# Optimization experiments

Hardware: AMD Instinct MI355X
Metric: run time of the kernel (lower is better)

## Reference

```python
import jax, jax.numpy as jnp
import numpy as np

D, H, E, K, DF = 1024, 16, 8, 2, 4096
HD = D // H


def setup_inputs() -> dict:
    key = jax.random.key(0)
    ks = jax.random.split(key, 16)
    s = 0.02
    return {
        "x": jax.random.normal(ks[0], (8, 1024, D), jnp.float32),
        "ln1_g": jnp.ones((D,), jnp.float32),
        "ln1_b": jnp.zeros((D,), jnp.float32),
        "Wqkv": jax.random.normal(ks[1], (D, 3 * D), jnp.float32) * s,
        "bqkv": jnp.zeros((3 * D,), jnp.float32),
        "Wo": jax.random.normal(ks[2], (D, D), jnp.float32) * s,
        "bo": jnp.zeros((D,), jnp.float32),
        "ln2_g": jnp.ones((D,), jnp.float32),
        "ln2_b": jnp.zeros((D,), jnp.float32),
        "Wr": jax.random.normal(ks[3], (D, E), jnp.float32) * s,
        "W1": jax.random.normal(ks[4], (E, D, DF), jnp.float32) * s,
        "b1": jnp.zeros((E, DF), jnp.float32),
        "W2": jax.random.normal(ks[5], (E, DF, D), jnp.float32) * s,
        "b2": jnp.zeros((E, D), jnp.float32),
    }


def _ln(x, g, b, eps=1e-5):
    mu = jnp.mean(x, axis=-1, keepdims=True)
    var = jnp.var(x, axis=-1, keepdims=True)
    return (x - mu) * jax.lax.rsqrt(var + eps) * g + b


def reference(x, ln1_g, ln1_b, Wqkv, bqkv, Wo, bo, ln2_g, ln2_b, Wr, W1, b1, W2, b2):
    B, S, _ = x.shape
    # ---- pre-norm multi-head attention ----
    n1 = _ln(x, ln1_g, ln1_b)
    qkv = n1 @ Wqkv + bqkv  # [B,S,3D]
    q, k, v = jnp.split(qkv, 3, axis=-1)
    q = q.reshape(B, S, H, HD).transpose(0, 2, 1, 3)
    k = k.reshape(B, S, H, HD).transpose(0, 2, 1, 3)
    v = v.reshape(B, S, H, HD).transpose(0, 2, 1, 3)
    scores = jnp.einsum("bhqd,bhkd->bhqk", q, k) / np.sqrt(HD).astype(np.float32)
    attn = jax.nn.softmax(scores, axis=-1)
    ao = jnp.einsum("bhqk,bhkd->bhqd", attn, v)
    ao = ao.transpose(0, 2, 1, 3).reshape(B, S, D) @ Wo + bo
    x = x + ao  # residual (dropout=0)

    # ---- pre-norm MoE FFN ----
    n2 = _ln(x, ln2_g, ln2_b).reshape(B * S, D)  # [T,D]
    logits = n2 @ Wr  # [T,E]
    probs = jax.nn.softmax(logits, axis=-1)
    topv, topi = jax.lax.top_k(probs, K)  # [T,K]
    topv = topv / jnp.sum(topv, axis=-1, keepdims=True)
    onehot = jax.nn.one_hot(topi, E, dtype=probs.dtype)  # [T,K,E]
    gates = jnp.einsum("tke,tk->te", onehot, topv)  # dense sparse gates [T,E]

    # dense dispatch: each expert's FFN weighted by its gate (zero for unrouted)
    moe = jnp.zeros_like(n2)
    for e in range(E):
        h = jax.nn.gelu(n2 @ W1[e] + b1[e])
        moe = moe + gates[:, e:e + 1] * (h @ W2[e] + b2[e])
    x = x + moe.reshape(B, S, D)

    # load-balancing aux loss: E * sum(frac_routed_e * mean_prob_e)
    frac = jnp.mean(jnp.sum(onehot, axis=1), axis=0) / K  # [E]
    aux = E * jnp.sum(frac * jnp.mean(probs, axis=0))
    return x, aux
```

## Files before the change

kernel.cpp:

```cpp
#include <hip/hip_runtime.h>
#include <cstdint>
#include <cstddef>

using u16 = unsigned short;
using u32 = unsigned int;
typedef __attribute__((ext_vector_type(8))) short bf16x8;
typedef __attribute__((ext_vector_type(4))) float f32x4;

#define T_TOK 8192
#define SEQ   1024
#define NHEAD 16

__device__ __forceinline__ u16 f2b(float f) {
  u32 u = __float_as_uint(f);
  u32 r = (u + 0x7FFFu + ((u >> 16) & 1u)) >> 16;
  return (u16)r;
}
__device__ __forceinline__ float b2f(u16 u) {
  return __uint_as_float(((u32)u) << 16);
}

__global__ __launch_bounds__(256)
void k_cast_transpose(const float* __restrict__ in, u16* __restrict__ out, int R, int C) {
  __shared__ float tile[32][33];
  int bc = blockIdx.x * 32, br = blockIdx.y * 32;
  size_t bofs = (size_t)blockIdx.z * R * C;
  in += bofs; out += bofs;
  int tx = threadIdx.x, ty = threadIdx.y;
  for (int i = 0; i < 32; i += 8)
    tile[ty + i][tx] = in[(size_t)(br + ty + i) * C + bc + tx];
  __syncthreads();
  for (int i = 0; i < 32; i += 8)
    out[(size_t)(bc + ty + i) * R + br + tx] = f2b(tile[tx][ty + i]);
}

__global__ __launch_bounds__(256)
void k_ln(const float* __restrict__ x, const float* __restrict__ g, const float* __restrict__ b,
          u16* __restrict__ out) {
  int row = blockIdx.x, t = threadIdx.x;
  float4 v = ((const float4*)(x + (size_t)row * 1024))[t];
  float s  = v.x + v.y + v.z + v.w;
  float ss = v.x * v.x + v.y * v.y + v.z * v.z + v.w * v.w;
  for (int d = 1; d < 64; d <<= 1) { s += __shfl_xor(s, d); ss += __shfl_xor(ss, d); }
  __shared__ float sm[8];
  int w = t >> 6, lane = t & 63;
  if (lane == 0) { sm[w] = s; sm[4 + w] = ss; }
  __syncthreads();
  s = sm[0] + sm[1] + sm[2] + sm[3];
  ss = sm[4] + sm[5] + sm[6] + sm[7];
  float mu = s * (1.f / 1024.f);
  float var = ss * (1.f / 1024.f) - mu * mu;
  float inv = rsqrtf(var + 1e-5f);
  float4 gv = ((const float4*)g)[t];
  float4 bv = ((const float4*)b)[t];
  u32 lo = (u32)f2b((v.x - mu) * inv * gv.x + bv.x) | ((u32)f2b((v.y - mu) * inv * gv.y + bv.y) << 16);
  u32 hi = (u32)f2b((v.z - mu) * inv * gv.z + bv.z) | ((u32)f2b((v.w - mu) * inv * gv.w + bv.w) << 16);
  u32* dst = (u32*)(out + (size_t)row * 1024 + t * 4);
  dst[0] = lo; dst[1] = hi;
}

template<int MODE, bool EXPERT, bool GATHER>
__global__ __launch_bounds__(256)
void k_gemm(const u16* __restrict__ A, const u16* __restrict__ BT,
            const float* __restrict__ bias, const float* __restrict__ res,
            void* __restrict__ Cout, int M, int N, int Kd, int ldA,
            const int* __restrict__ off, const int* __restrict__ rows) {
  int nx = gridDim.x;
  int rid = blockIdx.x + nx * (blockIdx.y + gridDim.y * blockIdx.z);
  int z, bx, by;
  if (EXPERT) {
    z = rid & 7;
    int inner = rid >> 3;
    bx = inner % nx;
    by = inner / nx;
  } else {
    z = 0;
    int xcd = rid & 7;
    int inner = rid >> 3;
    bx = inner % nx;
    by = (inner / nx) * 8 + xcd;
  }
  int m_base = 0, M_local = M;
  if (EXPERT) { m_base = off[z]; M_local = off[z + 1] - m_base; }
  if (by * 128 >= M_local) return;
  if (EXPERT) { BT += (size_t)z * N * Kd; bias += (size_t)z * N; }

  __shared__ alignas(1024) u16 As[2][4096];
  __shared__ alignas(1024) u16 Bs[2][4096];

  int t = threadIdx.x;
  int lane = t & 63, w = t >> 6;
  int wm = w >> 1, wn = w & 1;
  int lr = lane & 15;
  int slot = lane >> 4;
  int sx = (slot ^ ((lr >> 1) & 3)) << 3;

  int ssrc = (lane & 3) ^ ((lane >> 3) & 3);
  const u16* aG[2]; const u16* bG[2];
  u16* aL[2]; u16* bL[2];
#pragma unroll
  for (int c = 0; c < 2; c++) {
    int chunk = 2 * w + c;
    int rl = chunk * 16 + (lane >> 2);
    int mr = by * 128 + rl;
    int mc = mr < M_local - 1 ? mr : M_local - 1;
    size_t arow = GATHER ? (size_t)rows[m_base + mc] : (size_t)(m_base + mc);
    aG[c] = A + arow * (size_t)ldA + ssrc * 8;
    bG[c] = BT + (size_t)(bx * 128 + rl) * Kd + ssrc * 8;
    aL[c] = &As[0][chunk * 512];
    bL[c] = &Bs[0][chunk * 512];
  }

  auto stage = [&](int k0, int buf) {
#pragma unroll
    for (int c = 0; c < 2; c++) {
      __builtin_amdgcn_global_load_lds(
          (const __attribute__((address_space(1))) void*)(aG[c] + k0),
          (__attribute__((address_space(3))) void*)(aL[c] + buf * 4096), 16, 0, 0);
      __builtin_amdgcn_global_load_lds(
          (const __attribute__((address_space(1))) void*)(bG[c] + k0),
          (__attribute__((address_space(3))) void*)(bL[c] + buf * 4096), 16, 0, 0);
    }
  };

  f32x4 acc[4][4] = {};

  stage(0, 0);
  __syncthreads();
  int cur = 0;
  for (int k0 = 0; k0 < Kd; k0 += 32) {
    if (k0 + 32 < Kd) stage(k0 + 32, cur ^ 1);
    bf16x8 af[4], bfr[4];
#pragma unroll
    for (int m = 0; m < 4; m++)
      af[m] = *(const bf16x8*)&As[cur][(wm * 64 + m * 16 + lr) * 32 + sx];
#pragma unroll
    for (int n = 0; n < 4; n++)
      bfr[n] = *(const bf16x8*)&Bs[cur][(wn * 64 + n * 16 + lr) * 32 + sx];
#pragma unroll
    for (int m = 0; m < 4; m++)
#pragma unroll
      for (int n = 0; n < 4; n++)
        acc[m][n] = __builtin_amdgcn_mfma_f32_16x16x32_bf16(af[m], bfr[n], acc[m][n], 0, 0, 0);
    __syncthreads();
    cur ^= 1;
  }

  int cr = (lane >> 4) * 4, cc = lane & 15;
#pragma unroll
  for (int m = 0; m < 4; m++) {
    int rl = by * 128 + wm * 64 + m * 16 + cr;
#pragma unroll
    for (int n = 0; n < 4; n++) {
      int col = bx * 128 + wn * 64 + n * 16 + cc;
      float bia = bias[col];
#pragma unroll
      for (int r = 0; r < 4; r++) {
        int rr = rl + r;
        if (rr >= M_local) continue;
        size_t row = (size_t)(m_base + rr);
        float v = acc[m][n][r] + bia;
        if (MODE == 0) {
          ((u16*)Cout)[row * N + col] = f2b(v);
        } else if (MODE == 1) {
          ((float*)Cout)[row * N + col] = v + res[row * N + col];
        } else if (MODE == 2) {
          float u = v + 0.044715f * v * v * v;
          float ge = v / (1.f + __expf(-1.5957691216057308f * u));
          ((u16*)Cout)[row * N + col] = f2b(ge);
        } else {
          ((float*)Cout)[row * N + col] = v;
        }
      }
    }
  }
}

__global__ __launch_bounds__(256)
void k_attn(const u16* __restrict__ qkv, u16* __restrict__ ao) {
  __shared__ u16 Kt[64][72];
  __shared__ u16 Vt[64][72];
  __shared__ u16 Pl[4][16][72];

  int bh = blockIdx.y;
  int b = bh >> 4, h = bh & 15;
  int q0 = blockIdx.x * 64;
  int t = threadIdx.x, lane = t & 63, w = t >> 6;
  int lr = lane & 15, lk = (lane >> 4) * 8;

  int tq = b * SEQ + q0 + w * 16 + lr;
  const u16* qrow = qkv + (size_t)tq * 3072 + h * 64;
  bf16x8 qf[2];
#pragma unroll
  for (int kk = 0; kk < 2; kk++) {
    bf16x8 raw = *(const bf16x8*)(qrow + kk * 32 + lk);
#pragma unroll
    for (int j = 0; j < 8; j++) raw[j] = (short)f2b(b2f((u16)raw[j]) * 0.125f);
    qf[kk] = raw;
  }

  float m[4], l[4];
  f32x4 o[4];
#pragma unroll
  for (int r = 0; r < 4; r++) { m[r] = -1e30f; l[r] = 0.f; }
#pragma unroll
  for (int c = 0; c < 4; c++) o[c] = (f32x4){0.f, 0.f, 0.f, 0.f};

  int key_r = t >> 2;
  int key_c = (t & 3) * 16;

  for (int kv0 = 0; kv0 < SEQ; kv0 += 64) {
    int tk = b * SEQ + kv0 + key_r;
    const u16* krow = qkv + (size_t)tk * 3072 + 1024 + h * 64 + key_c;
    const u16* vrow = qkv + (size_t)tk * 3072 + 2048 + h * 64 + key_c;
    int4 ka = *(const int4*)krow;
    int4 kb = *(const int4*)(krow + 8);
    int4 vv4[2];
    vv4[0] = *(const int4*)vrow;
    vv4[1] = *(const int4*)(vrow + 8);
    const u16* vv = (const u16*)vv4;
    __syncthreads();
    *(int4*)&Kt[key_r][key_c] = ka;
    *(int4*)&Kt[key_r][key_c + 8] = kb;
#pragma unroll
    for (int j = 0; j < 16; j++) Vt[key_c + j][key_r] = vv[j];
    __syncthreads();

    f32x4 s[4];
#pragma unroll
    for (int n = 0; n < 4; n++) {
      s[n] = (f32x4){0.f, 0.f, 0.f, 0.f};
#pragma unroll
      for (int kk = 0; kk < 2; kk++) {
        bf16x8 kf = *(const bf16x8*)&Kt[n * 16 + lr][kk * 32 + lk];
        s[n] = __builtin_amdgcn_mfma_f32_16x16x32_bf16(qf[kk], kf, s[n], 0, 0, 0);
      }
    }
    float alpha[4], rsum[4];
#pragma unroll
    for (int r = 0; r < 4; r++) {
      float mx = fmaxf(fmaxf(s[0][r], s[1][r]), fmaxf(s[2][r], s[3][r]));
#pragma unroll
      for (int d = 1; d < 16; d <<= 1) mx = fmaxf(mx, __shfl_xor(mx, d));
      float mn = fmaxf(m[r], mx);
      alpha[r] = expf(m[r] - mn);
      m[r] = mn;
      rsum[r] = 0.f;
    }
#pragma unroll
    for (int n = 0; n < 4; n++)
#pragma unroll
      for (int r = 0; r < 4; r++) {
        float p = expf(s[n][r] - m[r]);
        rsum[r] += p;
        Pl[w][(lane >> 4) * 4 + r][n * 16 + lr] = f2b(p);
      }
#pragma unroll
    for (int r = 0; r < 4; r++) {
      float rs = rsum[r];
#pragma unroll
      for (int d = 1; d < 16; d <<= 1) rs += __shfl_xor(rs, d);
      l[r] = l[r] * alpha[r] + rs;
#pragma unroll
      for (int c = 0; c < 4; c++) o[c][r] *= alpha[r];
    }
    bf16x8 pa[2];
#pragma unroll
    for (int kk = 0; kk < 2; kk++) pa[kk] = *(const bf16x8*)&Pl[w][lr][kk * 32 + lk];
#pragma unroll
    for (int c = 0; c < 4; c++)
#pragma unroll
      for (int kk = 0; kk < 2; kk++) {
        bf16x8 vf = *(const bf16x8*)&Vt[c * 16 + lr][kk * 32 + lk];
        o[c] = __builtin_amdgcn_mfma_f32_16x16x32_bf16(pa[kk], vf, o[c], 0, 0, 0);
      }
  }

  int cr = (lane >> 4) * 4, cc = lane & 15;
#pragma unroll
  for (int r = 0; r < 4; r++) {
    float invl = 1.f / l[r];
    int trow = b * SEQ + q0 + w * 16 + cr + r;
#pragma unroll
    for (int c = 0; c < 4; c++)
      ao[(size_t)trow * 1024 + h * 64 + c * 16 + cc] = f2b(o[c][r] * invl);
  }
}

__global__ __launch_bounds__(256)
void k_router(const float* __restrict__ x1, const float* __restrict__ g, const float* __restrict__ b,
              const float* __restrict__ Wr, int* __restrict__ topi, float* __restrict__ topv,
              int* __restrict__ cnt_part, float* __restrict__ sp_part) {
  __shared__ int lcnt[8];
  __shared__ float lsp[8];
  int t = threadIdx.x, w = t >> 6, lane = t & 63;
  if (t < 8) { lcnt[t] = 0; lsp[t] = 0.f; }
  __syncthreads();

  float gv[16], bv[16];
#pragma unroll
  for (int i = 0; i < 4; i++) {
    float4 g4 = ((const float4*)g)[lane * 4 + i];
    float4 b4 = ((const float4*)b)[lane * 4 + i];
    gv[i * 4 + 0] = g4.x; gv[i * 4 + 1] = g4.y; gv[i * 4 + 2] = g4.z; gv[i * 4 + 3] = g4.w;
    bv[i * 4 + 0] = b4.x; bv[i * 4 + 1] = b4.y; bv[i * 4 + 2] = b4.z; bv[i * 4 + 3] = b4.w;
  }
  float wr[16][8];
#pragma unroll
  for (int j = 0; j < 16; j++) {
    float4 w0 = ((const float4*)Wr)[(lane * 16 + j) * 2];
    float4 w1 = ((const float4*)Wr)[(lane * 16 + j) * 2 + 1];
    wr[j][0] = w0.x; wr[j][1] = w0.y; wr[j][2] = w0.z; wr[j][3] = w0.w;
    wr[j][4] = w1.x; wr[j][5] = w1.y; wr[j][6] = w1.z; wr[j][7] = w1.w;
  }

  for (int i = 0; i < 8; i++) {
    int row = blockIdx.x * 32 + w * 8 + i;
    const float4* xr = (const float4*)(x1 + (size_t)row * 1024);
    float xv[16];
    float s = 0.f, ss = 0.f;
#pragma unroll
    for (int q = 0; q < 4; q++) {
      float4 v = xr[lane * 4 + q];
      xv[q * 4 + 0] = v.x; xv[q * 4 + 1] = v.y; xv[q * 4 + 2] = v.z; xv[q * 4 + 3] = v.w;
      s += v.x + v.y + v.z + v.w;
      ss += v.x * v.x + v.y * v.y + v.z * v.z + v.w * v.w;
    }
#pragma unroll
    for (int d = 1; d < 64; d <<= 1) { s += __shfl_xor(s, d); ss += __shfl_xor(ss, d); }
    float mu = s * (1.f / 1024.f);
    float var = ss * (1.f / 1024.f) - mu * mu;
    float inv = rsqrtf(var + 1e-5f);
    float p[8] = {};
#pragma unroll
    for (int j = 0; j < 16; j++) {
      float n = (xv[j] - mu) * inv * gv[j] + bv[j];
#pragma unroll
      for (int e = 0; e < 8; e++) p[e] += n * wr[j][e];
    }
#pragma unroll
    for (int e = 0; e < 8; e++)
#pragma unroll
      for (int d = 1; d < 64; d <<= 1) p[e] += __shfl_xor(p[e], d);
    if (lane == 0) {
      float mx = p[0];
#pragma unroll
      for (int e = 1; e < 8; e++) mx = fmaxf(mx, p[e]);
      float ex[8], sum = 0.f;
#pragma unroll
      for (int e = 0; e < 8; e++) { ex[e] = expf(p[e] - mx); sum += ex[e]; }
      float pr[8];
#pragma unroll
      for (int e = 0; e < 8; e++) pr[e] = ex[e] / sum;
      int i0 = 0; float b0 = pr[0];
      for (int e = 1; e < 8; e++) if (pr[e] > b0) { b0 = pr[e]; i0 = e; }
      int i1 = -1; float b1 = -1.f;
      for (int e = 0; e < 8; e++) if (e != i0 && pr[e] > b1) { b1 = pr[e]; i1 = e; }
      float inv2 = 1.f / (b0 + b1);
      topi[row * 2] = i0; topi[row * 2 + 1] = i1;
      topv[row * 2] = b0 * inv2; topv[row * 2 + 1] = b1 * inv2;
      atomicAdd(&lcnt[i0], 1); atomicAdd(&lcnt[i1], 1);
#pragma unroll
      for (int e = 0; e < 8; e++) atomicAdd(&lsp[e], pr[e]);
    }
  }
  __syncthreads();
  if (t < 8) {
    cnt_part[blockIdx.x * 8 + t] = lcnt[t];
    sp_part[blockIdx.x * 8 + t] = lsp[t];
  }
}

__global__ void k_scan_aux(const int* __restrict__ cnt_part, const float* __restrict__ sp_part,
                           int* __restrict__ off, int* __restrict__ cursor, float* __restrict__ aux_out) {
  __shared__ int csum[8];
  __shared__ float ssum[8];
  int t = threadIdx.x;
  int e = t & 7, ch = t >> 3;
  int c = 0; float s = 0.f;
  for (int i = ch * 32; i < ch * 32 + 32; i++) { c += cnt_part[i * 8 + e]; s += sp_part[i * 8 + e]; }
#pragma unroll
  for (int d = 8; d < 64; d <<= 1) { c += __shfl_xor(c, d); s += __shfl_xor(s, d); }
  if (t < 8) { csum[t] = c; ssum[t] = s; }
  __syncthreads();
  if (t == 0) {
    int o = 0;
    for (int q = 0; q < 8; q++) { off[q] = o; cursor[q] = o; o += csum[q]; }
    off[8] = o;
    float aux = 0.f;
    for (int q = 0; q < 8; q++)
      aux += ((float)csum[q] / (float)(T_TOK * 2)) * (ssum[q] / (float)T_TOK);
    aux_out[0] = 8.f * aux;
  }
}

__global__ __launch_bounds__(256)
void k_scatter(const int* __restrict__ topi, int* __restrict__ cursor,
               int* __restrict__ rows, int* __restrict__ slot_of) {
  __shared__ int hist[8];
  __shared__ int base[8];
  int t = threadIdx.x;
  if (t < 8) hist[t] = 0;
  __syncthreads();
  int tok = blockIdx.x * 256 + t;
  int e0 = topi[tok * 2], e1 = topi[tok * 2 + 1];
  int r0 = atomicAdd(&hist[e0], 1);
  int r1 = atomicAdd(&hist[e1], 1);
  __syncthreads();
  if (t < 8) base[t] = atomicAdd(&cursor[t], hist[t]);
  __syncthreads();
  int p0 = base[e0] + r0, p1 = base[e1] + r1;
  rows[p0] = tok; rows[p1] = tok;
  slot_of[tok * 2] = p0; slot_of[tok * 2 + 1] = p1;
}

__global__ __launch_bounds__(256)
void k_combine(const float* __restrict__ x1, const float* __restrict__ out2,
               const int* __restrict__ slot_of, const float* __restrict__ topv,
               float* __restrict__ out) {
  int row = blockIdx.x, t = threadIdx.x;
  int s0 = slot_of[row * 2], s1 = slot_of[row * 2 + 1];
  float w0 = topv[row * 2], w1 = topv[row * 2 + 1];
  float4 a  = ((const float4*)(x1 + (size_t)row * 1024))[t];
  float4 e0 = ((const float4*)(out2 + (size_t)s0 * 1024))[t];
  float4 e1 = ((const float4*)(out2 + (size_t)s1 * 1024))[t];
  float4 r;
  r.x = a.x + w0 * e0.x + w1 * e1.x;
  r.y = a.y + w0 * e0.y + w1 * e1.y;
  r.z = a.z + w0 * e0.z + w1 * e1.z;
  r.w = a.w + w0 * e0.w + w1 * e1.w;
  ((float4*)(out + (size_t)row * 1024))[t] = r;
}

extern "C" void kernel_launch(void* const* d_in, const int* in_sizes, int n_in,
                              void* d_out, int out_size, void* d_ws, size_t ws_size,
                              hipStream_t stream) {
  const float* x    = (const float*)d_in[0];
  const float* ln1g = (const float*)d_in[1];
  const float* ln1b = (const float*)d_in[2];
  const float* Wqkv = (const float*)d_in[3];
  const float* bqkv = (const float*)d_in[4];
  const float* Wo   = (const float*)d_in[5];
  const float* bo   = (const float*)d_in[6];
  const float* ln2g = (const float*)d_in[7];
  const float* ln2b = (const float*)d_in[8];
  const float* Wr   = (const float*)d_in[9];
  const float* W1   = (const float*)d_in[10];
  const float* b1   = (const float*)d_in[11];
  const float* W2   = (const float*)d_in[12];
  const float* b2   = (const float*)d_in[13];
  float* out = (float*)d_out;

  char* wp = (char*)d_ws;
  auto alloc = [&](size_t bytes) -> void* {
    void* p = (void*)wp;
    wp += (bytes + 255) & ~(size_t)255;
    return p;
  };
  u16*   WqkvT = (u16*)alloc((size_t)3072 * 1024 * 2);
  u16*   WoT   = (u16*)alloc((size_t)1024 * 1024 * 2);
  u16*   W1T   = (u16*)alloc((size_t)8 * 4096 * 1024 * 2);
  u16*   W2T   = (u16*)alloc((size_t)8 * 1024 * 4096 * 2);
  u16*   n1    = (u16*)alloc((size_t)8192 * 1024 * 2);
  u16*   qkv   = (u16*)alloc((size_t)8192 * 3072 * 2);
  u16*   aob   = (u16*)alloc((size_t)8192 * 1024 * 2);
  float* x1    = (float*)alloc((size_t)8192 * 1024 * 4);
  u16*   n2b   = (u16*)alloc((size_t)8192 * 1024 * 2);
  u16*   hbuf  = (u16*)alloc((size_t)16384 * 4096 * 2);
  float* out2  = (float*)alloc((size_t)16384 * 1024 * 4);
  int*   topi  = (int*)alloc((size_t)8192 * 2 * 4);
  float* topv  = (float*)alloc((size_t)8192 * 2 * 4);
  int*   rowsl = (int*)alloc((size_t)16384 * 4);
  int*   slot  = (int*)alloc((size_t)16384 * 4);
  int*   cntp  = (int*)alloc((size_t)256 * 8 * 4);
  float* spp   = (float*)alloc((size_t)256 * 8 * 4);
  int*   offs  = (int*)alloc(256);
  int*   curs  = (int*)alloc(256);

  k_cast_transpose<<<dim3(96, 32, 1), dim3(32, 8), 0, stream>>>(Wqkv, WqkvT, 1024, 3072);
  k_cast_transpose<<<dim3(32, 32, 1), dim3(32, 8), 0, stream>>>(Wo, WoT, 1024, 1024);
  k_cast_transpose<<<dim3(128, 32, 8), dim3(32, 8), 0, stream>>>(W1, W1T, 1024, 4096);
  k_cast_transpose<<<dim3(32, 128, 8), dim3(32, 8), 0, stream>>>(W2, W2T, 4096, 1024);

  k_ln<<<8192, 256, 0, stream>>>(x, ln1g, ln1b, n1);
  k_gemm<0, false, false><<<dim3(24, 64, 1), 256, 0, stream>>>(
      n1, WqkvT, bqkv, nullptr, qkv, 8192, 3072, 1024, 1024, nullptr, nullptr);
  k_attn<<<dim3(16, 128), 256, 0, stream>>>(qkv, aob);
  k_gemm<1, false, false><<<dim3(8, 64, 1), 256, 0, stream>>>(
      aob, WoT, bo, x, x1, 8192, 1024, 1024, 1024, nullptr, nullptr);

  k_ln<<<8192, 256, 0, stream>>>(x1, ln2g, ln2b, n2b);
  k_router<<<256, 256, 0, stream>>>(x1, ln2g, ln2b, Wr, topi, topv, cntp, spp);
  k_scan_aux<<<1, 64, 0, stream>>>(cntp, spp, offs, curs, out + 8388608);
  k_scatter<<<32, 256, 0, stream>>>(topi, curs, rowsl, slot);

  k_gemm<2, true, true><<<dim3(32, 64, 8), 256, 0, stream>>>(
      n2b, W1T, b1, nullptr, hbuf, 0, 4096, 1024, 1024, offs, rowsl);
  k_gemm<3, true, false><<<dim3(8, 64, 8), 256, 0, stream>>>(
      hbuf, W2T, b2, nullptr, out2, 0, 1024, 4096, 4096, offs, nullptr);
  k_combine<<<8192, 256, 0, stream>>>(x1, out2, slot, topv, out);
}
```

Measured before the change: 903.2 us.

## Triple-buffer GEMM LDS staging with explicit vmcnt waits and reorder expert tile mapping

Moves the GEMM mainloop from double to triple buffering in LDS. It replaces __syncthreads with raw s_barrier plus explicit s_waitcnt vmcnt counts, so two global-to-LDS loads stay in flight while each tile is computed. It also changes the expert GEMM block mapping so consecutive blocks walk the M dimension first, which changes reuse of expert weight tiles. The cost is more LDS per block, which may lower occupancy, and hand-written wait counts that must match the number of loads issued per stage.

```diff
diff --git a/kernel.cpp b/kernel.cpp
--- a/kernel.cpp
+++ b/kernel.cpp
@@ -65,14 +65,14 @@
             const float* __restrict__ bias, const float* __restrict__ res,
             void* __restrict__ Cout, int M, int N, int Kd, int ldA,
             const int* __restrict__ off, const int* __restrict__ rows) {
-  int nx = gridDim.x;
-  int rid = blockIdx.x + nx * (blockIdx.y + gridDim.y * blockIdx.z);
+  int nx = gridDim.x, ny = gridDim.y;
+  int rid = blockIdx.x + nx * (blockIdx.y + ny * blockIdx.z);
   int z, bx, by;
   if (EXPERT) {
     z = rid & 7;
     int inner = rid >> 3;
-    bx = inner % nx;
-    by = inner / nx;
+    by = inner % ny;
+    bx = inner / ny;
   } else {
     z = 0;
     int xcd = rid & 7;
@@ -85,8 +85,8 @@
   if (by * 128 >= M_local) return;
   if (EXPERT) { BT += (size_t)z * N * Kd; bias += (size_t)z * N; }
 
-  __shared__ alignas(1024) u16 As[2][4096];
-  __shared__ alignas(1024) u16 Bs[2][4096];
+  __shared__ alignas(1024) u16 As[3][4096];
+  __shared__ alignas(1024) u16 Bs[3][4096];
 
   int t = threadIdx.x;
   int lane = t & 63, w = t >> 6;
@@ -97,7 +97,7 @@
 
   int ssrc = (lane & 3) ^ ((lane >> 3) & 3);
   const u16* aG[2]; const u16* bG[2];
-  u16* aL[2]; u16* bL[2];
+  int cofs[2];
 #pragma unroll
   for (int c = 0; c < 2; c++) {
     int chunk = 2 * w + c;
@@ -107,29 +107,26 @@
     size_t arow = GATHER ? (size_t)rows[m_base + mc] : (size_t)(m_base + mc);
     aG[c] = A + arow * (size_t)ldA + ssrc * 8;
     bG[c] = BT + (size_t)(bx * 128 + rl) * Kd + ssrc * 8;
-    aL[c] = &As[0][chunk * 512];
-    bL[c] = &Bs[0][chunk * 512];
-  }
-
-  auto stage = [&](int k0, int buf) {
+    cofs[c] = chunk * 512;
+  }
+
+  auto stage = [&](int s) {
+    int k0 = s * 32;
+    int buf = s % 3;
 #pragma unroll
     for (int c = 0; c < 2; c++) {
       __builtin_amdgcn_global_load_lds(
           (const __attribute__((address_space(1))) void*)(aG[c] + k0),
-          (__attribute__((address_space(3))) void*)(aL[c] + buf * 4096), 16, 0, 0);
+          (__attribute__((address_space(3))) void*)(&As[buf][cofs[c]]), 16, 0, 0);
       __builtin_amdgcn_global_load_lds(
           (const __attribute__((address_space(1))) void*)(bG[c] + k0),
-          (__attribute__((address_space(3))) void*)(bL[c] + buf * 4096), 16, 0, 0);
+          (__attribute__((address_space(3))) void*)(&Bs[buf][cofs[c]]), 16, 0, 0);
     }
   };
 
   f32x4 acc[4][4] = {};
 
-  stage(0, 0);
-  __syncthreads();
-  int cur = 0;
-  for (int k0 = 0; k0 < Kd; k0 += 32) {
-    if (k0 + 32 < Kd) stage(k0 + 32, cur ^ 1);
+  auto compute = [&](int cur) {
     bf16x8 af[4], bfr[4];
 #pragma unroll
     for (int m = 0; m < 4; m++)
@@ -142,9 +139,23 @@
 #pragma unroll
       for (int n = 0; n < 4; n++)
         acc[m][n] = __builtin_amdgcn_mfma_f32_16x16x32_bf16(af[m], bfr[n], acc[m][n], 0, 0, 0);
-    __syncthreads();
-    cur ^= 1;
-  }
+  };
+
+  int nsteps = Kd >> 5;
+  stage(0); stage(1);
+  for (int k = 0; k < nsteps - 2; ++k) {
+    __builtin_amdgcn_s_barrier();
+    stage(k + 2);
+    asm volatile("s_waitcnt vmcnt(8)" ::: "memory");
+    __builtin_amdgcn_s_barrier();
+    compute(k % 3);
+  }
+  asm volatile("s_waitcnt vmcnt(4)" ::: "memory");
+  __builtin_amdgcn_s_barrier();
+  compute((nsteps - 2) % 3);
+  asm volatile("s_waitcnt vmcnt(0)" ::: "memory");
+  __builtin_amdgcn_s_barrier();
+  compute((nsteps - 1) % 3);
 
   int cr = (lane >> 4) * 4, cc = lane & 15;
 #pragma unroll
```

Result: slower. 979.5 us (+8.5%).
